# Kernel tuning notes

Hardware: AMD Instinct MI355X
Metric: run time of the kernel (lower is better)

Reference implementation:

```python
import jax, jax.numpy as jnp
import numpy as np

N, C, R, G = 500000, 256, 64, 4096

def setup_inputs() -> dict:
    key = jax.random.key(0)
    k1, k2, k3, k4 = jax.random.split(key, 4)
    x = jax.random.normal(k1, (N, C), dtype=jnp.float32)
    batch = jnp.sort(jax.random.randint(k2, (N,), 0, G, dtype=jnp.int64))
    # Kaiming-ish small init for the bias-free MLP weights (torch layout: [out, in])
    w1 = jax.random.normal(k3, (R, C), dtype=jnp.float32) * (1.0 / np.sqrt(C))
    w2 = jax.random.normal(k4, (C, R), dtype=jnp.float32) * (1.0 / np.sqrt(R))
    return {"x": x, "batch": batch, "w1": w1, "w2": w2, "size": G}

def _mlp(z, w1, w2):
    # Linear(C->C/r, no bias) -> ReLU -> Linear(C/r->C, no bias)
    h = jax.nn.relu(jnp.einsum('gc,rc->gr', z, w1))
    return jnp.einsum('gr,cr->gc', h, w2)

def reference(x, batch, w1, w2, size):
    # segment max / sum pooling over graphs ([N,C] -> [G,C])
    max_res = jax.ops.segment_max(x, batch, num_segments=size, indices_are_sorted=True)
    # torch_scatter fills empty segments with 0 for 'max'
    max_res = jnp.where(jnp.isneginf(max_res), 0.0, max_res)
    sum_res = jax.ops.segment_sum(x, batch, num_segments=size, indices_are_sorted=True)
    y = jax.nn.sigmoid(_mlp(max_res, w1, w2) + _mlp(sum_res, w1, w2))  # [G,C]
    return x * y[batch]  # gather-broadcast multiply back to nodes
```

## Files before the change

kernel.cpp:

```cpp
#include <hip/hip_runtime.h>
#include <cfloat>
#include <math.h>

#define N_NODES 500000
#define C_DIM   256
#define R_DIM   64
#define G_NUM   4096

__global__ __launch_bounds__(256) void seg_pool_kernel(
    const float* __restrict__ x, const int* __restrict__ batch,
    float* __restrict__ gmax, float* __restrict__ gsum) {
  const int g = blockIdx.x;

  int lo = 0, hi = N_NODES;
  while (lo < hi) { int mid = (lo + hi) >> 1; if (batch[mid] < g) lo = mid + 1; else hi = mid; }
  const int start = lo;
  hi = N_NODES;
  while (lo < hi) { int mid = (lo + hi) >> 1; if (batch[mid] <= g) lo = mid + 1; else hi = mid; }
  const int end = lo;

  const int tid = threadIdx.x;
  const int c4  = tid & 63;
  const int rg  = tid >> 6;

  float4 vmax = make_float4(-FLT_MAX, -FLT_MAX, -FLT_MAX, -FLT_MAX);
  float4 vsum = make_float4(0.f, 0.f, 0.f, 0.f);

  const float4* xr = (const float4*)x;
  for (int n = start + rg; n < end; n += 4) {
    float4 v = xr[(size_t)n * 64 + c4];
    vmax.x = fmaxf(vmax.x, v.x); vmax.y = fmaxf(vmax.y, v.y);
    vmax.z = fmaxf(vmax.z, v.z); vmax.w = fmaxf(vmax.w, v.w);
    vsum.x += v.x; vsum.y += v.y; vsum.z += v.z; vsum.w += v.w;
  }

  __shared__ float4 smax[4][64];
  __shared__ float4 ssum[4][64];
  smax[rg][c4] = vmax;
  ssum[rg][c4] = vsum;
  __syncthreads();

  if (rg == 0) {
    for (int i = 1; i < 4; ++i) {
      float4 m = smax[i][c4];
      float4 s = ssum[i][c4];
      vmax.x = fmaxf(vmax.x, m.x); vmax.y = fmaxf(vmax.y, m.y);
      vmax.z = fmaxf(vmax.z, m.z); vmax.w = fmaxf(vmax.w, m.w);
      vsum.x += s.x; vsum.y += s.y; vsum.z += s.z; vsum.w += s.w;
    }
    if (start == end) vmax = make_float4(0.f, 0.f, 0.f, 0.f);
    ((float4*)gmax)[(size_t)g * 64 + c4] = vmax;
    ((float4*)gsum)[(size_t)g * 64 + c4] = vsum;
  }
}

__global__ __launch_bounds__(256) void mlp_kernel(
    const float* __restrict__ gmax, const float* __restrict__ gsum,
    const float* __restrict__ w1, const float* __restrict__ w2,
    float* __restrict__ y) {
  const int g   = blockIdx.x;
  const int tid = threadIdx.x;

  __shared__ float zm[C_DIM];
  __shared__ float zs[C_DIM];
  __shared__ float red_m[256];
  __shared__ float red_s[256];
  __shared__ float hs[R_DIM];

  zm[tid] = gmax[(size_t)g * C_DIM + tid];
  zs[tid] = gsum[(size_t)g * C_DIM + tid];
  __syncthreads();

  const int r    = tid & 63;
  const int part = tid >> 6;
  float pm = 0.f, ps = 0.f;
  const float* w1r = w1 + (size_t)r * C_DIM + part * 64;
  const float* zmp = zm + part * 64;
  const float* zsp = zs + part * 64;
#pragma unroll 8
  for (int c = 0; c < 64; ++c) {
    float w = w1r[c];
    pm += w * zmp[c];
    ps += w * zsp[c];
  }
  red_m[tid] = pm;
  red_s[tid] = ps;
  __syncthreads();
  if (part == 0) {
    float am = pm + red_m[64 + r] + red_m[128 + r] + red_m[192 + r];
    float as = ps + red_s[64 + r] + red_s[128 + r] + red_s[192 + r];
    hs[r] = fmaxf(am, 0.f) + fmaxf(as, 0.f);
  }
  __syncthreads();

  float acc = 0.f;
  const float4* w2c = (const float4*)(w2 + (size_t)tid * R_DIM);
#pragma unroll
  for (int q = 0; q < R_DIM / 4; ++q) {
    float4 w = w2c[q];
    acc += w.x * hs[4 * q + 0] + w.y * hs[4 * q + 1] +
           w.z * hs[4 * q + 2] + w.w * hs[4 * q + 3];
  }
  y[(size_t)g * C_DIM + tid] = 1.f / (1.f + expf(-acc));
}

__global__ __launch_bounds__(256) void apply_kernel(
    const float* __restrict__ x, const int* __restrict__ batch,
    const float* __restrict__ y, float* __restrict__ out) {
  const long long idx = (long long)blockIdx.x * 256 + threadIdx.x;
  if (idx >= (long long)N_NODES * 64) return;
  const int n   = (int)(idx >> 6);
  const int rem = (int)(idx & 63);
  const int b   = batch[n];
  float4 xv = ((const float4*)x)[idx];
  float4 yv = ((const float4*)y)[(size_t)b * 64 + rem];
  float4 o;
  o.x = xv.x * yv.x; o.y = xv.y * yv.y; o.z = xv.z * yv.z; o.w = xv.w * yv.w;
  ((float4*)out)[idx] = o;
}

extern "C" void kernel_launch(void* const* d_in, const int* in_sizes, int n_in,
                              void* d_out, int out_size, void* d_ws, size_t ws_size,
                              hipStream_t stream) {
  const float* x     = (const float*)d_in[0];
  const int*   batch = (const int*)d_in[1];
  const float* w1    = (const float*)d_in[2];
  const float* w2    = (const float*)d_in[3];
  float* out = (float*)d_out;

  float* gmax = (float*)d_ws;
  float* gsum = gmax + (size_t)G_NUM * C_DIM;
  float* y    = gsum + (size_t)G_NUM * C_DIM;

  seg_pool_kernel<<<G_NUM, 256, 0, stream>>>(x, batch, gmax, gsum);
  mlp_kernel<<<G_NUM, 256, 0, stream>>>(gmax, gsum, w1, w2, y);

  const int n4 = N_NODES * (C_DIM / 4);
  apply_kernel<<<(n4 + 255) / 256, 256, 0, stream>>>(x, batch, y, out);
}
```

Before: 960.1 us.

## Fuse segment pooling, MLP, and gather-multiply into one per-graph kernel

Merges the three kernels into one block-per-graph kernel. Each block pools its segment, runs the small MLP from shared memory, then rescales its own rows of x and writes out with nontemporal loads and stores. This drops the global gmax/gsum/y round-trips, two launches, and the per-element batch gather. The second read of each segment's x may hit in cache shortly after pooling. The risk is that per-graph work (about 122 rows) gives uneven load and serialises the phases within each block.

```diff
diff --git a/kernel.cpp b/kernel.cpp
--- a/kernel.cpp
+++ b/kernel.cpp
@@ -7,9 +7,12 @@
 #define R_DIM   64
 #define G_NUM   4096
 
-__global__ __launch_bounds__(256) void seg_pool_kernel(
+typedef float f32x4 __attribute__((ext_vector_type(4)));
+
+__global__ __launch_bounds__(256) void fused_kernel(
     const float* __restrict__ x, const int* __restrict__ batch,
-    float* __restrict__ gmax, float* __restrict__ gsum) {
+    const float* __restrict__ w1, const float* __restrict__ w2,
+    float* __restrict__ out) {
   const int g = blockIdx.x;
 
   int lo = 0, hi = N_NODES;
@@ -18,105 +21,92 @@
   hi = N_NODES;
   while (lo < hi) { int mid = (lo + hi) >> 1; if (batch[mid] <= g) lo = mid + 1; else hi = mid; }
   const int end = lo;
+  if (end == start) return;
 
   const int tid = threadIdx.x;
   const int c4  = tid & 63;
   const int rg  = tid >> 6;
 
-  float4 vmax = make_float4(-FLT_MAX, -FLT_MAX, -FLT_MAX, -FLT_MAX);
-  float4 vsum = make_float4(0.f, 0.f, 0.f, 0.f);
+  __shared__ f32x4 smax[4][64];
+  __shared__ f32x4 ssum[4][64];
+  __shared__ float zm[C_DIM];
+  __shared__ float zs[C_DIM];
+  __shared__ float red_m[256];
+  __shared__ float red_s[256];
+  __shared__ float hs[R_DIM];
+  __shared__ float yl[C_DIM];
 
-  const float4* xr = (const float4*)x;
+  f32x4 vmax = { -FLT_MAX, -FLT_MAX, -FLT_MAX, -FLT_MAX };
+  f32x4 vsum = { 0.f, 0.f, 0.f, 0.f };
+  const f32x4* __restrict__ xr = (const f32x4*)x;
   for (int n = start + rg; n < end; n += 4) {
-    float4 v = xr[(size_t)n * 64 + c4];
+    f32x4 v = xr[(size_t)n * 64 + c4];
     vmax.x = fmaxf(vmax.x, v.x); vmax.y = fmaxf(vmax.y, v.y);
     vmax.z = fmaxf(vmax.z, v.z); vmax.w = fmaxf(vmax.w, v.w);
-    vsum.x += v.x; vsum.y += v.y; vsum.z += v.z; vsum.w += v.w;
+    vsum += v;
   }
-
-  __shared__ float4 smax[4][64];
-  __shared__ float4 ssum[4][64];
   smax[rg][c4] = vmax;
   ssum[rg][c4] = vsum;
   __syncthreads();
 
   if (rg == 0) {
     for (int i = 1; i < 4; ++i) {
-      float4 m = smax[i][c4];
-      float4 s = ssum[i][c4];
+      f32x4 m = smax[i][c4];
       vmax.x = fmaxf(vmax.x, m.x); vmax.y = fmaxf(vmax.y, m.y);
       vmax.z = fmaxf(vmax.z, m.z); vmax.w = fmaxf(vmax.w, m.w);
-      vsum.x += s.x; vsum.y += s.y; vsum.z += s.z; vsum.w += s.w;
+      vsum += ssum[i][c4];
     }
-    if (start == end) vmax = make_float4(0.f, 0.f, 0.f, 0.f);
-    ((float4*)gmax)[(size_t)g * 64 + c4] = vmax;
-    ((float4*)gsum)[(size_t)g * 64 + c4] = vsum;
-  }
-}
-
-__global__ __launch_bounds__(256) void mlp_kernel(
-    const float* __restrict__ gmax, const float* __restrict__ gsum,
-    const float* __restrict__ w1, const float* __restrict__ w2,
-    float* __restrict__ y) {
-  const int g   = blockIdx.x;
-  const int tid = threadIdx.x;
-
-  __shared__ float zm[C_DIM];
-  __shared__ float zs[C_DIM];
-  __shared__ float red_m[256];
-  __shared__ float red_s[256];
-  __shared__ float hs[R_DIM];
-
-  zm[tid] = gmax[(size_t)g * C_DIM + tid];
-  zs[tid] = gsum[(size_t)g * C_DIM + tid];
-  __syncthreads();
-
-  const int r    = tid & 63;
-  const int part = tid >> 6;
-  float pm = 0.f, ps = 0.f;
-  const float* w1r = w1 + (size_t)r * C_DIM + part * 64;
-  const float* zmp = zm + part * 64;
-  const float* zsp = zs + part * 64;
-#pragma unroll 8
-  for (int c = 0; c < 64; ++c) {
-    float w = w1r[c];
-    pm += w * zmp[c];
-    ps += w * zsp[c];
-  }
-  red_m[tid] = pm;
-  red_s[tid] = ps;
-  __syncthreads();
-  if (part == 0) {
-    float am = pm + red_m[64 + r] + red_m[128 + r] + red_m[192 + r];
-    float as = ps + red_s[64 + r] + red_s[128 + r] + red_s[192 + r];
-    hs[r] = fmaxf(am, 0.f) + fmaxf(as, 0.f);
+    ((f32x4*)zm)[c4] = vmax;
+    ((f32x4*)zs)[c4] = vsum;
   }
   __syncthreads();
 
-  float acc = 0.f;
-  const float4* w2c = (const float4*)(w2 + (size_t)tid * R_DIM);
+  {
+    const int r    = tid & 63;
+    const int part = tid >> 6;
+    float pm = 0.f, ps = 0.f;
+    const float* w1r = w1 + (size_t)r * C_DIM + part * 64;
+    const float* zmp = zm + part * 64;
+    const float* zsp = zs + part * 64;
+#pragma unroll 8
+    for (int c = 0; c < 64; ++c) {
+      float w = w1r[c];
+      pm += w * zmp[c];
+      ps += w * zsp[c];
+    }
+    red_m[tid] = pm;
+    red_s[tid] = ps;
+    __syncthreads();
+    if (part == 0) {
+      float am = pm + red_m[64 + r] + red_m[128 + r] + red_m[192 + r];
+      float as = ps + red_s[64 + r] + red_s[128 + r] + red_s[192 + r];
+      hs[r] = fmaxf(am, 0.f) + fmaxf(as, 0.f);
+    }
+    __syncthreads();
+  }
+
+  {
+    float acc = 0.f;
+    const f32x4* w2c = (const f32x4*)(w2 + (size_t)tid * R_DIM);
 #pragma unroll
-  for (int q = 0; q < R_DIM / 4; ++q) {
-    float4 w = w2c[q];
-    acc += w.x * hs[4 * q + 0] + w.y * hs[4 * q + 1] +
-           w.z * hs[4 * q + 2] + w.w * hs[4 * q + 3];
+    for (int q = 0; q < R_DIM / 4; ++q) {
+      f32x4 w = w2c[q];
+      acc += w.x * hs[4 * q + 0] + w.y * hs[4 * q + 1] +
+             w.z * hs[4 * q + 2] + w.w * hs[4 * q + 3];
+    }
+    yl[tid] = 1.f / (1.f + expf(-acc));
   }
-  y[(size_t)g * C_DIM + tid] = 1.f / (1.f + expf(-acc));
-}
+  __syncthreads();
 
-__global__ __launch_bounds__(256) void apply_kernel(
-    const float* __restrict__ x, const int* __restrict__ batch,
-    const float* __restrict__ y, float* __restrict__ out) {
-  const long long idx = (long long)blockIdx.x * 256 + threadIdx.x;
-  if (idx >= (long long)N_NODES * 64) return;
-  const int n   = (int)(idx >> 6);
-  const int rem = (int)(idx & 63);
-  const int b   = batch[n];
-  float4 xv = ((const float4*)x)[idx];
-  float4 yv = ((const float4*)y)[(size_t)b * 64 + rem];
-  float4 o;
-  o.x = xv.x * yv.x; o.y = xv.y * yv.y; o.z = xv.z * yv.z; o.w = xv.w * yv.w;
-  ((float4*)out)[idx] = o;
+  {
+    const f32x4 y4 = ((const f32x4*)yl)[c4];
+    f32x4* outr = (f32x4*)out;
+    for (int n = start + rg; n < end; n += 4) {
+      f32x4 v = __builtin_nontemporal_load(&xr[(size_t)n * 64 + c4]);
+      v *= y4;
+      __builtin_nontemporal_store(v, &outr[(size_t)n * 64 + c4]);
+    }
+  }
 }
 
 extern "C" void kernel_launch(void* const* d_in, const int* in_sizes, int n_in,
@@ -127,14 +117,7 @@
   const float* w1    = (const float*)d_in[2];
   const float* w2    = (const float*)d_in[3];
   float* out = (float*)d_out;
+  (void)d_ws; (void)ws_size;
 
-  float* gmax = (float*)d_ws;
-  float* gsum = gmax + (size_t)G_NUM * C_DIM;
-  float* y    = gsum + (size_t)G_NUM * C_DIM;
-
-  seg_pool_kernel<<<G_NUM, 256, 0, stream>>>(x, batch, gmax, gsum);
-  mlp_kernel<<<G_NUM, 256, 0, stream>>>(gmax, gsum, w1, w2, y);
-
-  const int n4 = N_NODES * (C_DIM / 4);
-  apply_kernel<<<(n4 + 255) / 256, 256, 0, stream>>>(x, batch, y, out);
+  fused_kernel<<<G_NUM, 256, 0, stream>>>(x, batch, w1, w2, out);
 }
```

Measured after the change: 921.6 us. 1.04x faster.
